# Kernel tuning notes

Hardware: AMD Instinct MI355X
Metric: run time of the kernel (lower is better)

Reference implementation:

```python
import jax, jax.numpy as jnp
import numpy as np

N_NODES = 50000
N_EDGES = 1_600_000
IN_DIM = 64
HID_DIM = 64
OUT_DIM = 64


def setup_inputs() -> dict:
    key = jax.random.key(0)
    k = jax.random.split(key, 7)
    feat = jax.random.normal(k[0], (N_NODES, IN_DIM), dtype=jnp.float32)
    src = jax.random.randint(k[1], (N_EDGES,), 0, N_NODES, dtype=jnp.int32)
    dst = jax.random.randint(k[2], (N_EDGES,), 0, N_NODES, dtype=jnp.int32)
    # nn.init.normal_(weight, std=0.1); bias default uniform ~ small, use 0.1*randn
    W1 = 0.1 * jax.random.normal(k[3], (HID_DIM, IN_DIM), dtype=jnp.float32)
    b1 = 0.1 * jax.random.normal(k[4], (HID_DIM,), dtype=jnp.float32)
    W2 = 0.1 * jax.random.normal(k[5], (OUT_DIM, HID_DIM), dtype=jnp.float32)
    b2 = 0.1 * jax.random.normal(k[6], (OUT_DIM,), dtype=jnp.float32)
    return {"feat": feat, "src": src, "dst": dst, "W1": W1, "b1": b1, "W2": W2, "b2": b2}


def _gnn_layer(h, src, dst, W, b):
    # copy_u + sum: gather source-node features along edges, scatter-sum to dst
    agg = jax.ops.segment_sum(h[src], dst, num_segments=N_NODES)  # [N, d_in]
    return agg @ W.T + b  # nn.Linear


def reference(feat, src, dst, W1, b1, W2, b2):
    h = _gnn_layer(feat, src, dst, W1, b1)
    h = jnp.tanh(h)
    h = _gnn_layer(h, src, dst, W2, b2)
    return h
```

## Files before the change

kernel.cpp:

```cpp
#include <hip/hip_runtime.h>

#define N_NODES 50000
#define N_EDGES 1600000
#define DIM 64
#define NBK 196
#define BIN_BLOCKS 391
#define CSR_CAP 12288
#define QCAP 3072

__device__ __forceinline__ unsigned short f2bf(float f) {
    union { float f; unsigned u; } v; v.f = f;
    unsigned r = v.u + 0x7FFF + ((v.u >> 16) & 1);
    return (unsigned short)(r >> 16);
}
__device__ __forceinline__ float bf2f(unsigned short h) {
    union { unsigned u; float f; } v; v.u = ((unsigned)h) << 16;
    return v.f;
}

__global__ __launch_bounds__(256) void init_bcur(int* __restrict__ bcur) {
    if (threadIdx.x < NBK) bcur[threadIdx.x * 16] = threadIdx.x * CSR_CAP;
}

__global__ __launch_bounds__(256) void bin_edges(const int* __restrict__ src,
                                                 const int* __restrict__ dst,
                                                 int* __restrict__ bcur,
                                                 int* __restrict__ binned) {
    __shared__ int cnt[NBK];
    __shared__ int lofs[NBK];
    __shared__ int shiftv[NBK];
    __shared__ int sb[256];
    __shared__ int stag[4096];
    __shared__ unsigned char stb[4096];
    int tid = threadIdx.x;
    if (tid < NBK) cnt[tid] = 0;
    __syncthreads();

    int base = blockIdx.x * 4096;
    int nedge = N_EDGES - base;
    if (nedge > 4096) nedge = 4096;

    int myb[16], myr[16], myp[16];
#pragma unroll
    for (int i = 0; i < 16; ++i) {
        int e = base + i * 256 + tid;
        myb[i] = -1;
        if (e < N_EDGES) {
            int s = src[e], d = dst[e];
            int b = d >> 8;
            myb[i] = b;
            myp[i] = ((d & 255) << 16) | s;
            myr[i] = atomicAdd(&cnt[b], 1);
        }
    }
    __syncthreads();

    int c = (tid < NBK) ? cnt[tid] : 0;
    sb[tid] = c;
    __syncthreads();
    for (int off = 1; off < 256; off <<= 1) {
        int u = (tid >= off) ? sb[tid - off] : 0;
        __syncthreads();
        sb[tid] += u;
        __syncthreads();
    }
    if (tid < NBK) {
        lofs[tid] = sb[tid] - c;
        if (c) shiftv[tid] = atomicAdd(&bcur[tid * 16], c) - lofs[tid];
    }
    __syncthreads();

#pragma unroll
    for (int i = 0; i < 16; ++i) {
        if (myb[i] >= 0) {
            int idx = lofs[myb[i]] + myr[i];
            stag[idx] = myp[i];
            stb[idx] = (unsigned char)myb[i];
        }
    }
    __syncthreads();

    for (int i = tid; i < nedge; i += 256)
        binned[i + shiftv[stb[i]]] = stag[i];
}

__global__ __launch_bounds__(256) void build_csr(const int* __restrict__ binned,
                                                 const int* __restrict__ bcur,
                                                 unsigned* __restrict__ nodeinfo,
                                                 unsigned short* __restrict__ csr16) {
    __shared__ int cnt[64], cnt2[64], ofs[64], pcs[64], sb[64];
    __shared__ int qtot;
    int tid = threadIdx.x;
    int b = blockIdx.x >> 2;
    int q = blockIdx.x & 3;
    int ibase = b * CSR_CAP;
    int qbase = (b * 4 + q) * QCAP;
    int m = bcur[b * 16] - ibase;
    if (m > CSR_CAP) m = CSR_CAP;
    if (tid < 64) { cnt[tid] = 0; cnt2[tid] = 0; }
    __syncthreads();

    for (int i = tid; i < m; i += 256) {
        int dl = (binned[ibase + i] >> 16) & 255;
        if ((dl >> 6) == q) atomicAdd(&cnt[dl & 63], 1);
    }
    __syncthreads();

    int v = 0;
    if (tid < 64) {
        v = (cnt[tid] + 7) & ~7;
        pcs[tid] = v;
        sb[tid] = v;
    }
    __syncthreads();
    for (int off = 1; off < 64; off <<= 1) {
        int u = (tid >= off && tid < 64) ? sb[tid - off] : 0;
        __syncthreads();
        if (tid < 64) sb[tid] += u;
        __syncthreads();
    }
    if (tid < 64) {
        ofs[tid] = sb[tid] - v;
        int node = (b << 8) + (q << 6) + tid;
        if (node < N_NODES)
            nodeinfo[node] = ((unsigned)v << 23) | (unsigned)(qbase + ofs[tid]);
    }
    if (tid == 63) qtot = sb[63];
    __syncthreads();

    int qt = qtot;
    for (int i = tid; i < qt; i += 256) csr16[qbase + i] = (unsigned short)N_NODES;
    __syncthreads();

    for (int i = tid; i < m; i += 256) {
        int p = binned[ibase + i];
        int dl = (p >> 16) & 255;
        if ((dl >> 6) == q) {
            int r = atomicAdd(&cnt2[dl & 63], 1);
            csr16[qbase + ofs[dl & 63] + r] = (unsigned short)(p & 0xFFFF);
        }
    }
}

__global__ __launch_bounds__(256) void gemm64_f32(const float* __restrict__ X,
                                                  const float* __restrict__ W,
                                                  unsigned short* __restrict__ T,
                                                  int n_rows) {
    __shared__ float Ws[64 * 64];
    int tid = threadIdx.x;
#pragma unroll
    for (int j = 0; j < 16; ++j) Ws[j * 256 + tid] = W[j * 256 + tid];
    __syncthreads();

    int n = blockIdx.x * 256 + tid;
    if (n >= n_rows) {
        if (n == n_rows) {
            ushort4 z = {0, 0, 0, 0};
            ushort4* tp = (ushort4*)(T + (size_t)n * 64);
#pragma unroll
            for (int k = 0; k < 16; ++k) tp[k] = z;
        }
        return;
    }

    float4 x[16];
    const float4* xp = (const float4*)(X + (size_t)n * 64);
#pragma unroll
    for (int k = 0; k < 16; ++k) x[k] = xp[k];

    ushort4* tp = (ushort4*)(T + (size_t)n * 64);
    for (int fg = 0; fg < 16; ++fg) {
        float r[4];
#pragma unroll
        for (int fi = 0; fi < 4; ++fi) {
            int f = fg * 4 + fi;
            float acc = 0.f;
#pragma unroll
            for (int k4 = 0; k4 < 16; ++k4) {
                float4 w = *(const float4*)&Ws[f * 64 + k4 * 4];
                float4 xv = x[k4];
                acc += xv.x * w.x + xv.y * w.y + xv.z * w.z + xv.w * w.w;
            }
            r[fi] = acc;
        }
        ushort4 o;
        o.x = f2bf(r[0]); o.y = f2bf(r[1]); o.z = f2bf(r[2]); o.w = f2bf(r[3]);
        tp[fg] = o;
    }
}

__global__ __launch_bounds__(256) void gemm64_bf16(const unsigned short* __restrict__ X,
                                                   const float* __restrict__ W,
                                                   unsigned short* __restrict__ T,
                                                   int n_rows) {
    __shared__ float Ws[64 * 64];
    int tid = threadIdx.x;
#pragma unroll
    for (int j = 0; j < 16; ++j) Ws[j * 256 + tid] = W[j * 256 + tid];
    __syncthreads();

    int n = blockIdx.x * 256 + tid;
    if (n >= n_rows) {
        if (n == n_rows) {
            ushort4 z = {0, 0, 0, 0};
            ushort4* tp = (ushort4*)(T + (size_t)n * 64);
#pragma unroll
            for (int k = 0; k < 16; ++k) tp[k] = z;
        }
        return;
    }

    uint4 xr[8];
    const uint4* xp = (const uint4*)(X + (size_t)n * 64);
#pragma unroll
    for (int k = 0; k < 8; ++k) xr[k] = xp[k];
    float x[64];
    const unsigned* xu = (const unsigned*)xr;
#pragma unroll
    for (int p = 0; p < 32; ++p) {
        unsigned u = xu[p];
        union { unsigned u; float f; } lo, hi;
        lo.u = u << 16;
        hi.u = u & 0xFFFF0000u;
        x[2 * p] = lo.f;
        x[2 * p + 1] = hi.f;
    }

    const float4* xv4 = (const float4*)x;
    ushort4* tp = (ushort4*)(T + (size_t)n * 64);
    for (int fg = 0; fg < 16; ++fg) {
        float r[4];
#pragma unroll
        for (int fi = 0; fi < 4; ++fi) {
            int f = fg * 4 + fi;
            float acc = 0.f;
#pragma unroll
            for (int k4 = 0; k4 < 16; ++k4) {
                float4 w = *(const float4*)&Ws[f * 64 + k4 * 4];
                float4 xv = xv4[k4];
                acc += xv.x * w.x + xv.y * w.y + xv.z * w.z + xv.w * w.w;
            }
            r[fi] = acc;
        }
        ushort4 o;
        o.x = f2bf(r[0]); o.y = f2bf(r[1]); o.z = f2bf(r[2]); o.w = f2bf(r[3]);
        tp[fg] = o;
    }
}

__global__ __launch_bounds__(256) void aggregate(const unsigned short* __restrict__ T,
                                                 const unsigned short* __restrict__ csr,
                                                 const unsigned* __restrict__ nodeinfo,
                                                 const float* __restrict__ bias,
                                                 void* __restrict__ outp,
                                                 int mode) {
    int node = blockIdx.x * 4 + (threadIdx.x >> 6);
    int lane = threadIdx.x & 63;
    if (node >= N_NODES) return;
    unsigned info = nodeinfo[node];
    int pos = (int)(info & 0x7FFFFFu);
    int pcnt = (int)(info >> 23);
    const uint4* ix = (const uint4*)(csr + pos);
    float acc = bias[lane];
    int groups = pcnt >> 3;
    if (groups) {
        uint4 iv = ix[0];
        for (int g = 0; g < groups; ++g) {
            uint4 ivn;
            if (g + 1 < groups) ivn = ix[g + 1];
            int s0 = iv.x & 0xFFFF, s1 = iv.x >> 16;
            int s2 = iv.y & 0xFFFF, s3 = iv.y >> 16;
            int s4 = iv.z & 0xFFFF, s5 = iv.z >> 16;
            int s6 = iv.w & 0xFFFF, s7 = iv.w >> 16;
            unsigned short v0 = T[(size_t)s0 * DIM + lane];
            unsigned short v1 = T[(size_t)s1 * DIM + lane];
            unsigned short v2 = T[(size_t)s2 * DIM + lane];
            unsigned short v3 = T[(size_t)s3 * DIM + lane];
            unsigned short v4 = T[(size_t)s4 * DIM + lane];
            unsigned short v5 = T[(size_t)s5 * DIM + lane];
            unsigned short v6 = T[(size_t)s6 * DIM + lane];
            unsigned short v7 = T[(size_t)s7 * DIM + lane];
            acc += (bf2f(v0) + bf2f(v1)) + (bf2f(v2) + bf2f(v3)) +
                   (bf2f(v4) + bf2f(v5)) + (bf2f(v6) + bf2f(v7));
            iv = ivn;
        }
    }
    if (mode) {
        float e = __expf(2.f * acc);
        acc = 1.f - 2.f / (e + 1.f);
        ((unsigned short*)outp)[(size_t)node * DIM + lane] = f2bf(acc);
    } else {
        ((float*)outp)[(size_t)node * DIM + lane] = acc;
    }
}

extern "C" void kernel_launch(void* const* d_in, const int* in_sizes, int n_in,
                              void* d_out, int out_size, void* d_ws, size_t ws_size,
                              hipStream_t stream) {
    const float* feat = (const float*)d_in[0];
    const int*   src  = (const int*)d_in[1];
    const int*   dst  = (const int*)d_in[2];
    const float* W1   = (const float*)d_in[3];
    const float* b1   = (const float*)d_in[4];
    const float* W2   = (const float*)d_in[5];
    const float* b2   = (const float*)d_in[6];

    int*            binned   = (int*)d_ws;
    unsigned short* csr16    = (unsigned short*)(binned + NBK * CSR_CAP);
    unsigned*       nodeinfo = (unsigned*)(csr16 + NBK * CSR_CAP);
    int*            bcur     = (int*)(nodeinfo + N_NODES);
    unsigned short* t        = (unsigned short*)(bcur + NBK * 16 + 8);

    unsigned short* h = (unsigned short*)d_out;
    float* out = (float*)d_out;

    const int NB = (N_NODES + 3) / 4;
    const int GB = (N_NODES + 256) / 256;

    init_bcur<<<1, 256, 0, stream>>>(bcur);
    bin_edges<<<BIN_BLOCKS, 256, 0, stream>>>(src, dst, bcur, binned);
    build_csr<<<NBK * 4, 256, 0, stream>>>(binned, bcur, nodeinfo, csr16);

    gemm64_f32<<<GB, 256, 0, stream>>>(feat, W1, t, N_NODES);
    aggregate<<<NB, 256, 0, stream>>>(t, csr16, nodeinfo, b1, h, 1);

    gemm64_bf16<<<GB, 256, 0, stream>>>(h, W2, t, N_NODES);
    aggregate<<<NB, 256, 0, stream>>>(t, csr16, nodeinfo, b2, out, 0);
}
```

Measured before the change: 252.6 us.

## Use 64-node CSR buckets and 16-byte vector gathers in aggregation

Edge binning now uses 782 buckets of 64 destination nodes instead of 196 buckets of 256, so build_csr runs one block per bucket and no longer scans each bucket four times with a quarter filter. The aggregate kernel now has each group of 8 lanes gather a full 16-byte slice of one source row, covering 8 edges at once, and then reduces across lanes with xor shuffles. This replaces eight 2-byte scalar loads per lane with one vector load, cutting memory transactions per edge at the cost of shuffle reductions. The workspace is reordered so the feature table comes first, which keeps its rows 16-byte aligned.

```diff
diff --git a/kernel.cpp b/kernel.cpp
--- a/kernel.cpp
+++ b/kernel.cpp
@@ -3,79 +3,99 @@
 #define N_NODES 50000
 #define N_EDGES 1600000
 #define DIM 64
-#define NBK 196
-#define BIN_BLOCKS 391
-#define CSR_CAP 12288
-#define QCAP 3072
+#define SBK 782
+#define SCAP 2560
+#define BIN_EPB 2048
+#define BIN_BLOCKS 782
 
 __device__ __forceinline__ unsigned short f2bf(float f) {
     union { float f; unsigned u; } v; v.f = f;
     unsigned r = v.u + 0x7FFF + ((v.u >> 16) & 1);
     return (unsigned short)(r >> 16);
 }
-__device__ __forceinline__ float bf2f(unsigned short h) {
-    union { unsigned u; float f; } v; v.u = ((unsigned)h) << 16;
-    return v.f;
+__device__ __forceinline__ float bf_lo(unsigned u) {
+    union { unsigned u; float f; } v; v.u = u << 16;  return v.f;
+}
+__device__ __forceinline__ float bf_hi(unsigned u) {
+    union { unsigned u; float f; } v; v.u = u & 0xFFFF0000u;  return v.f;
 }
 
 __global__ __launch_bounds__(256) void init_bcur(int* __restrict__ bcur) {
-    if (threadIdx.x < NBK) bcur[threadIdx.x * 16] = threadIdx.x * CSR_CAP;
+    for (int i = threadIdx.x; i < SBK; i += 256) bcur[i * 16] = i * SCAP;
 }
 
 __global__ __launch_bounds__(256) void bin_edges(const int* __restrict__ src,
                                                  const int* __restrict__ dst,
                                                  int* __restrict__ bcur,
                                                  int* __restrict__ binned) {
-    __shared__ int cnt[NBK];
-    __shared__ int lofs[NBK];
-    __shared__ int shiftv[NBK];
-    __shared__ int sb[256];
-    __shared__ int stag[4096];
-    __shared__ unsigned char stb[4096];
+    __shared__ int cnt[SBK];
+    __shared__ int lofs[SBK];
+    __shared__ int shiftv[SBK];
+    __shared__ int csum[256];
+    __shared__ int stag[BIN_EPB];
+    __shared__ unsigned short stb[BIN_EPB];
     int tid = threadIdx.x;
-    if (tid < NBK) cnt[tid] = 0;
-    __syncthreads();
-
-    int base = blockIdx.x * 4096;
+    for (int i = tid; i < SBK; i += 256) cnt[i] = 0;
+    __syncthreads();
+
+    int base = blockIdx.x * BIN_EPB;
     int nedge = N_EDGES - base;
-    if (nedge > 4096) nedge = 4096;
-
-    int myb[16], myr[16], myp[16];
-#pragma unroll
-    for (int i = 0; i < 16; ++i) {
+    if (nedge > BIN_EPB) nedge = BIN_EPB;
+
+    int myb[8], myr[8], myp[8];
+#pragma unroll
+    for (int i = 0; i < 8; ++i) {
         int e = base + i * 256 + tid;
         myb[i] = -1;
         if (e < N_EDGES) {
             int s = src[e], d = dst[e];
-            int b = d >> 8;
+            int b = d >> 6;
             myb[i] = b;
-            myp[i] = ((d & 255) << 16) | s;
+            myp[i] = ((d & 63) << 16) | s;
             myr[i] = atomicAdd(&cnt[b], 1);
         }
     }
     __syncthreads();
 
-    int c = (tid < NBK) ? cnt[tid] : 0;
-    sb[tid] = c;
+    int c4[4] = {0, 0, 0, 0};
+    int own = 0;
+    if (tid < 196) {
+#pragma unroll
+        for (int j = 0; j < 4; ++j) {
+            int idx = tid * 4 + j;
+            if (idx < SBK) { c4[j] = cnt[idx]; own += c4[j]; }
+        }
+    }
+    csum[tid] = own;
     __syncthreads();
     for (int off = 1; off < 256; off <<= 1) {
-        int u = (tid >= off) ? sb[tid - off] : 0;
+        int u = (tid >= off) ? csum[tid - off] : 0;
         __syncthreads();
-        sb[tid] += u;
+        csum[tid] += u;
         __syncthreads();
     }
-    if (tid < NBK) {
-        lofs[tid] = sb[tid] - c;
-        if (c) shiftv[tid] = atomicAdd(&bcur[tid * 16], c) - lofs[tid];
-    }
-    __syncthreads();
-
-#pragma unroll
-    for (int i = 0; i < 16; ++i) {
+    if (tid < 196) {
+        int run = csum[tid] - own;
+#pragma unroll
+        for (int j = 0; j < 4; ++j) {
+            int idx = tid * 4 + j;
+            if (idx < SBK) { lofs[idx] = run; run += c4[j]; }
+        }
+    }
+    __syncthreads();
+
+    for (int i = tid; i < SBK; i += 256) {
+        int c = cnt[i];
+        if (c) shiftv[i] = atomicAdd(&bcur[i * 16], c) - lofs[i];
+    }
+    __syncthreads();
+
+#pragma unroll
+    for (int i = 0; i < 8; ++i) {
         if (myb[i] >= 0) {
             int idx = lofs[myb[i]] + myr[i];
             stag[idx] = myp[i];
-            stb[idx] = (unsigned char)myb[i];
+            stb[idx] = (unsigned short)myb[i];
         }
     }
     __syncthreads();
@@ -88,30 +108,22 @@
                                                  const int* __restrict__ bcur,
                                                  unsigned* __restrict__ nodeinfo,
                                                  unsigned short* __restrict__ csr16) {
-    __shared__ int cnt[64], cnt2[64], ofs[64], pcs[64], sb[64];
+    __shared__ int cnt[64], cnt2[64], ofs[64], sb[64];
     __shared__ int qtot;
     int tid = threadIdx.x;
-    int b = blockIdx.x >> 2;
-    int q = blockIdx.x & 3;
-    int ibase = b * CSR_CAP;
-    int qbase = (b * 4 + q) * QCAP;
+    int b = blockIdx.x;
+    int ibase = b * SCAP;
     int m = bcur[b * 16] - ibase;
-    if (m > CSR_CAP) m = CSR_CAP;
+    if (m > SCAP) m = SCAP;
     if (tid < 64) { cnt[tid] = 0; cnt2[tid] = 0; }
     __syncthreads();
 
-    for (int i = tid; i < m; i += 256) {
-        int dl = (binned[ibase + i] >> 16) & 255;
-        if ((dl >> 6) == q) atomicAdd(&cnt[dl & 63], 1);
-    }
+    for (int i = tid; i < m; i += 256)
+        atomicAdd(&cnt[binned[ibase + i] >> 16], 1);
     __syncthreads();
 
     int v = 0;
-    if (tid < 64) {
-        v = (cnt[tid] + 7) & ~7;
-        pcs[tid] = v;
-        sb[tid] = v;
-    }
+    if (tid < 64) { v = (cnt[tid] + 7) & ~7; sb[tid] = v; }
     __syncthreads();
     for (int off = 1; off < 64; off <<= 1) {
         int u = (tid >= off && tid < 64) ? sb[tid - off] : 0;
@@ -121,24 +133,22 @@
     }
     if (tid < 64) {
         ofs[tid] = sb[tid] - v;
-        int node = (b << 8) + (q << 6) + tid;
+        int node = (b << 6) + tid;
         if (node < N_NODES)
-            nodeinfo[node] = ((unsigned)v << 23) | (unsigned)(qbase + ofs[tid]);
+            nodeinfo[node] = ((unsigned)v << 22) | (unsigned)(ibase + ofs[tid]);
     }
     if (tid == 63) qtot = sb[63];
     __syncthreads();
 
     int qt = qtot;
-    for (int i = tid; i < qt; i += 256) csr16[qbase + i] = (unsigned short)N_NODES;
+    for (int i = tid; i < qt; i += 256) csr16[ibase + i] = (unsigned short)N_NODES;
     __syncthreads();
 
     for (int i = tid; i < m; i += 256) {
         int p = binned[ibase + i];
-        int dl = (p >> 16) & 255;
-        if ((dl >> 6) == q) {
-            int r = atomicAdd(&cnt2[dl & 63], 1);
-            csr16[qbase + ofs[dl & 63] + r] = (unsigned short)(p & 0xFFFF);
-        }
+        int dl = p >> 16;
+        int r = atomicAdd(&cnt2[dl], 1);
+        csr16[ibase + ofs[dl] + r] = (unsigned short)(p & 0xFFFF);
     }
 }
 
@@ -219,11 +229,8 @@
 #pragma unroll
     for (int p = 0; p < 32; ++p) {
         unsigned u = xu[p];
-        union { unsigned u; float f; } lo, hi;
-        lo.u = u << 16;
-        hi.u = u & 0xFFFF0000u;
-        x[2 * p] = lo.f;
-        x[2 * p + 1] = hi.f;
+        x[2 * p] = bf_lo(u);
+        x[2 * p + 1] = bf_hi(u);
     }
 
     const float4* xv4 = (const float4*)x;
@@ -258,39 +265,52 @@
     int lane = threadIdx.x & 63;
     if (node >= N_NODES) return;
     unsigned info = nodeinfo[node];
-    int pos = (int)(info & 0x7FFFFFu);
-    int pcnt = (int)(info >> 23);
+    int pos = (int)(info & 0x3FFFFFu);
+    int groups = (int)(info >> 22) >> 3;
+    int q = lane >> 3;
+    int fl = lane & 7;
     const uint4* ix = (const uint4*)(csr + pos);
-    float acc = bias[lane];
-    int groups = pcnt >> 3;
+    const char* Tb = (const char*)T;
+    int fb = fl * 16;
+
+    float a0 = 0.f, a1 = 0.f, a2 = 0.f, a3 = 0.f,
+          a4 = 0.f, a5 = 0.f, a6 = 0.f, a7 = 0.f;
     if (groups) {
         uint4 iv = ix[0];
         for (int g = 0; g < groups; ++g) {
             uint4 ivn;
             if (g + 1 < groups) ivn = ix[g + 1];
-            int s0 = iv.x & 0xFFFF, s1 = iv.x >> 16;
-            int s2 = iv.y & 0xFFFF, s3 = iv.y >> 16;
-            int s4 = iv.z & 0xFFFF, s5 = iv.z >> 16;
-            int s6 = iv.w & 0xFFFF, s7 = iv.w >> 16;
-            unsigned short v0 = T[(size_t)s0 * DIM + lane];
-            unsigned short v1 = T[(size_t)s1 * DIM + lane];
-            unsigned short v2 = T[(size_t)s2 * DIM + lane];
-            unsigned short v3 = T[(size_t)s3 * DIM + lane];
-            unsigned short v4 = T[(size_t)s4 * DIM + lane];
-            unsigned short v5 = T[(size_t)s5 * DIM + lane];
-            unsigned short v6 = T[(size_t)s6 * DIM + lane];
-            unsigned short v7 = T[(size_t)s7 * DIM + lane];
-            acc += (bf2f(v0) + bf2f(v1)) + (bf2f(v2) + bf2f(v3)) +
-                   (bf2f(v4) + bf2f(v5)) + (bf2f(v6) + bf2f(v7));
+            unsigned w = (q & 2) ? ((q & 4) ? iv.w : iv.y)
+                                 : ((q & 4) ? iv.z : iv.x);
+            unsigned s = (q & 1) ? (w >> 16) : (w & 0xFFFFu);
+            uint4 r = *(const uint4*)(Tb + (size_t)s * 128 + fb);
+            a0 += bf_lo(r.x); a1 += bf_hi(r.x);
+            a2 += bf_lo(r.y); a3 += bf_hi(r.y);
+            a4 += bf_lo(r.z); a5 += bf_hi(r.z);
+            a6 += bf_lo(r.w); a7 += bf_hi(r.w);
             iv = ivn;
         }
     }
+#pragma unroll
+    for (int mask = 8; mask <= 32; mask <<= 1) {
+        a0 += __shfl_xor(a0, mask, 64);
+        a1 += __shfl_xor(a1, mask, 64);
+        a2 += __shfl_xor(a2, mask, 64);
+        a3 += __shfl_xor(a3, mask, 64);
+        a4 += __shfl_xor(a4, mask, 64);
+        a5 += __shfl_xor(a5, mask, 64);
+        a6 += __shfl_xor(a6, mask, 64);
+        a7 += __shfl_xor(a7, mask, 64);
+    }
+    int col = fl * 8 + q;
+    float av[8] = {a0, a1, a2, a3, a4, a5, a6, a7};
+    float a = av[q] + bias[col];
     if (mode) {
-        float e = __expf(2.f * acc);
-        acc = 1.f - 2.f / (e + 1.f);
-        ((unsigned short*)outp)[(size_t)node * DIM + lane] = f2bf(acc);
+        float e = __expf(2.f * a);
+        a = 1.f - 2.f / (e + 1.f);
+        ((unsigned short*)outp)[(size_t)node * DIM + col] = f2bf(a);
     } else {
-        ((float*)outp)[(size_t)node * DIM + lane] = acc;
+        ((float*)outp)[(size_t)node * DIM + col] = a;
     }
 }
 
@@ -305,11 +325,11 @@
     const float* W2   = (const float*)d_in[5];
     const float* b2   = (const float*)d_in[6];
 
-    int*            binned   = (int*)d_ws;
-    unsigned short* csr16    = (unsigned short*)(binned + NBK * CSR_CAP);
-    unsigned*       nodeinfo = (unsigned*)(csr16 + NBK * CSR_CAP);
+    unsigned short* t        = (unsigned short*)d_ws;
+    int*            binned   = (int*)(t + (size_t)(N_NODES + 1) * 64);
+    unsigned short* csr16    = (unsigned short*)(binned + SBK * SCAP);
+    unsigned*       nodeinfo = (unsigned*)(csr16 + SBK * SCAP);
     int*            bcur     = (int*)(nodeinfo + N_NODES);
-    unsigned short* t        = (unsigned short*)(bcur + NBK * 16 + 8);
 
     unsigned short* h = (unsigned short*)d_out;
     float* out = (float*)d_out;
@@ -319,7 +339,7 @@
 
     init_bcur<<<1, 256, 0, stream>>>(bcur);
     bin_edges<<<BIN_BLOCKS, 256, 0, stream>>>(src, dst, bcur, binned);
-    build_csr<<<NBK * 4, 256, 0, stream>>>(binned, bcur, nodeinfo, csr16);
+    build_csr<<<SBK, 256, 0, stream>>>(binned, bcur, nodeinfo, csr16);
 
     gemm64_f32<<<GB, 256, 0, stream>>>(feat, W1, t, N_NODES);
     aggregate<<<NB, 256, 0, stream>>>(t, csr16, nodeinfo, b1, h, 1);
```

Result: slower. 266.6 us (+5.5%).

## Gather 16-byte feature chunks per lane in aggregate and reduce via wave shuffles

Applied to the files above, without the earlier changes.

The aggregate kernel now assigns each lane one of the 8 edges in a group and one 16-byte slice of the source row, so each lane does a single uint4 load instead of eight scalar 2-byte loads. Partial sums for the 8 features in that slice are combined across edge lanes with xor shuffles, and then each lane picks one output column. The aim is to cut the number of memory instructions and make gather loads wider, at the cost of shuffle reductions and a strided output column mapping. The workspace offset for nodeinfo is also corrected to match the csr16 size, and an unused shared array is removed.

```diff
diff --git a/kernel.cpp b/kernel.cpp
--- a/kernel.cpp
+++ b/kernel.cpp
@@ -13,9 +13,11 @@
     unsigned r = v.u + 0x7FFF + ((v.u >> 16) & 1);
     return (unsigned short)(r >> 16);
 }
-__device__ __forceinline__ float bf2f(unsigned short h) {
-    union { unsigned u; float f; } v; v.u = ((unsigned)h) << 16;
-    return v.f;
+__device__ __forceinline__ float bf_lo(unsigned u) {
+    union { unsigned u; float f; } v; v.u = u << 16;  return v.f;
+}
+__device__ __forceinline__ float bf_hi(unsigned u) {
+    union { unsigned u; float f; } v; v.u = u & 0xFFFF0000u;  return v.f;
 }
 
 __global__ __launch_bounds__(256) void init_bcur(int* __restrict__ bcur) {
@@ -88,7 +90,7 @@
                                                  const int* __restrict__ bcur,
                                                  unsigned* __restrict__ nodeinfo,
                                                  unsigned short* __restrict__ csr16) {
-    __shared__ int cnt[64], cnt2[64], ofs[64], pcs[64], sb[64];
+    __shared__ int cnt[64], cnt2[64], ofs[64], sb[64];
     __shared__ int qtot;
     int tid = threadIdx.x;
     int b = blockIdx.x >> 2;
@@ -107,11 +109,7 @@
     __syncthreads();
 
     int v = 0;
-    if (tid < 64) {
-        v = (cnt[tid] + 7) & ~7;
-        pcs[tid] = v;
-        sb[tid] = v;
-    }
+    if (tid < 64) { v = (cnt[tid] + 7) & ~7; sb[tid] = v; }
     __syncthreads();
     for (int off = 1; off < 64; off <<= 1) {
         int u = (tid >= off && tid < 64) ? sb[tid - off] : 0;
@@ -219,11 +217,8 @@
 #pragma unroll
     for (int p = 0; p < 32; ++p) {
         unsigned u = xu[p];
-        union { unsigned u; float f; } lo, hi;
-        lo.u = u << 16;
-        hi.u = u & 0xFFFF0000u;
-        x[2 * p] = lo.f;
-        x[2 * p + 1] = hi.f;
+        x[2 * p] = bf_lo(u);
+        x[2 * p + 1] = bf_hi(u);
     }
 
     const float4* xv4 = (const float4*)x;
@@ -259,38 +254,52 @@
     if (node >= N_NODES) return;
     unsigned info = nodeinfo[node];
     int pos = (int)(info & 0x7FFFFFu);
-    int pcnt = (int)(info >> 23);
+    int groups = (int)(info >> 23) >> 3;
+    int q = lane >> 3;
+    int fl = lane & 7;
     const uint4* ix = (const uint4*)(csr + pos);
-    float acc = bias[lane];
-    int groups = pcnt >> 3;
+    const char* Tb = (const char*)T;
+    int fb = fl * 16;
+
+    float a0 = 0.f, a1 = 0.f, a2 = 0.f, a3 = 0.f,
+          a4 = 0.f, a5 = 0.f, a6 = 0.f, a7 = 0.f;
     if (groups) {
         uint4 iv = ix[0];
         for (int g = 0; g < groups; ++g) {
             uint4 ivn;
             if (g + 1 < groups) ivn = ix[g + 1];
-            int s0 = iv.x & 0xFFFF, s1 = iv.x >> 16;
-            int s2 = iv.y & 0xFFFF, s3 = iv.y >> 16;
-            int s4 = iv.z & 0xFFFF, s5 = iv.z >> 16;
-            int s6 = iv.w & 0xFFFF, s7 = iv.w >> 16;
-            unsigned short v0 = T[(size_t)s0 * DIM + lane];
-            unsigned short v1 = T[(size_t)s1 * DIM + lane];
-            unsigned short v2 = T[(size_t)s2 * DIM + lane];
-            unsigned short v3 = T[(size_t)s3 * DIM + lane];
-            unsigned short v4 = T[(size_t)s4 * DIM + lane];
-            unsigned short v5 = T[(size_t)s5 * DIM + lane];
-            unsigned short v6 = T[(size_t)s6 * DIM + lane];
-            unsigned short v7 = T[(size_t)s7 * DIM + lane];
-            acc += (bf2f(v0) + bf2f(v1)) + (bf2f(v2) + bf2f(v3)) +
-                   (bf2f(v4) + bf2f(v5)) + (bf2f(v6) + bf2f(v7));
+            unsigned w = (q & 2) ? ((q & 4) ? iv.w : iv.y)
+                                 : ((q & 4) ? iv.z : iv.x);
+            unsigned s = (q & 1) ? (w >> 16) : (w & 0xFFFFu);
+            uint4 r = *(const uint4*)(Tb + (size_t)s * 128 + fb);
+            a0 += bf_lo(r.x); a1 += bf_hi(r.x);
+            a2 += bf_lo(r.y); a3 += bf_hi(r.y);
+            a4 += bf_lo(r.z); a5 += bf_hi(r.z);
+            a6 += bf_lo(r.w); a7 += bf_hi(r.w);
             iv = ivn;
         }
     }
+#pragma unroll
+    for (int mask = 8; mask <= 32; mask <<= 1) {
+        a0 += __shfl_xor(a0, mask, 64);
+        a1 += __shfl_xor(a1, mask, 64);
+        a2 += __shfl_xor(a2, mask, 64);
+        a3 += __shfl_xor(a3, mask, 64);
+        a4 += __shfl_xor(a4, mask, 64);
+        a5 += __shfl_xor(a5, mask, 64);
+        a6 += __shfl_xor(a6, mask, 64);
+        a7 += __shfl_xor(a7, mask, 64);
+    }
+    float a = (q < 4) ? ((q < 2) ? (q == 0 ? a0 : a1) : (q == 2 ? a2 : a3))
+                      : ((q < 6) ? (q == 4 ? a4 : a5) : (q == 6 ? a6 : a7));
+    int col = fl * 8 + q;
+    a += bias[col];
     if (mode) {
-        float e = __expf(2.f * acc);
-        acc = 1.f - 2.f / (e + 1.f);
-        ((unsigned short*)outp)[(size_t)node * DIM + lane] = f2bf(acc);
+        float e = __expf(2.f * a);
+        a = 1.f - 2.f / (e + 1.f);
+        ((unsigned short*)outp)[(size_t)node * DIM + col] = f2bf(a);
     } else {
-        ((float*)outp)[(size_t)node * DIM + lane] = acc;
+        ((float*)outp)[(size_t)node * DIM + col] = a;
     }
 }
 
@@ -307,7 +316,7 @@
 
     int*            binned   = (int*)d_ws;
     unsigned short* csr16    = (unsigned short*)(binned + NBK * CSR_CAP);
-    unsigned*       nodeinfo = (unsigned*)(csr16 + NBK * CSR_CAP);
+    unsigned*       nodeinfo = (unsigned*)(csr16 + NBK * 4 * QCAP);
     int*            bcur     = (int*)(nodeinfo + N_NODES);
     unsigned short* t        = (unsigned short*)(bcur + NBK * 16 + 8);
 
```

Measured after the change: 259.9 us. +2.9%, slower.

## Fuse edge binning with first GEMM and unroll aggregation by sixteen edges

Applied to the files above, without the earlier changes.

Merges the edge-binning kernel and the first feature GEMM into one launch, with extra blocks taking the GEMM role, so the two independent stages run concurrently. The bcur init kernel becomes a memset, with the bin base offset added inside the kernel. Node edge lists are padded to multiples of 16 so the aggregation loop can issue 16 gathers per iteration into two accumulators, raising memory-level parallelism. The fused kernel's shared memory grows by the 16KB weight tile for all blocks, which may lower occupancy of the binning blocks, and padding adds more dummy gathers.

```diff
diff --git a/kernel.cpp b/kernel.cpp
--- a/kernel.cpp
+++ b/kernel.cpp
@@ -7,32 +7,80 @@
 #define BIN_BLOCKS 391
 #define CSR_CAP 12288
 #define QCAP 3072
+#define GEMM_BLOCKS 197
 
 __device__ __forceinline__ unsigned short f2bf(float f) {
     union { float f; unsigned u; } v; v.f = f;
     unsigned r = v.u + 0x7FFF + ((v.u >> 16) & 1);
     return (unsigned short)(r >> 16);
 }
+__device__ __forceinline__ float bf_lo(unsigned u) {
+    union { unsigned u; float f; } v; v.u = u << 16;  return v.f;
+}
+__device__ __forceinline__ float bf_hi(unsigned u) {
+    union { unsigned u; float f; } v; v.u = u & 0xFFFF0000u;  return v.f;
+}
 __device__ __forceinline__ float bf2f(unsigned short h) {
-    union { unsigned u; float f; } v; v.u = ((unsigned)h) << 16;
-    return v.f;
-}
-
-__global__ __launch_bounds__(256) void init_bcur(int* __restrict__ bcur) {
-    if (threadIdx.x < NBK) bcur[threadIdx.x * 16] = threadIdx.x * CSR_CAP;
-}
-
-__global__ __launch_bounds__(256) void bin_edges(const int* __restrict__ src,
-                                                 const int* __restrict__ dst,
-                                                 int* __restrict__ bcur,
-                                                 int* __restrict__ binned) {
+    union { unsigned u; float f; } v; v.u = ((unsigned)h) << 16;  return v.f;
+}
+
+__global__ __launch_bounds__(256) void bin_and_gemm1(const int* __restrict__ src,
+                                                     const int* __restrict__ dst,
+                                                     int* __restrict__ bcur,
+                                                     int* __restrict__ binned,
+                                                     const float* __restrict__ X,
+                                                     const float* __restrict__ W,
+                                                     unsigned short* __restrict__ T) {
     __shared__ int cnt[NBK];
     __shared__ int lofs[NBK];
     __shared__ int shiftv[NBK];
     __shared__ int sb[256];
     __shared__ int stag[4096];
     __shared__ unsigned char stb[4096];
+    __shared__ float Ws[64 * 64];
     int tid = threadIdx.x;
+
+    if (blockIdx.x >= BIN_BLOCKS) {
+#pragma unroll
+        for (int j = 0; j < 16; ++j) Ws[j * 256 + tid] = W[j * 256 + tid];
+        __syncthreads();
+
+        int n = (blockIdx.x - BIN_BLOCKS) * 256 + tid;
+        if (n > N_NODES) return;
+        ushort4* tp = (ushort4*)(T + (size_t)n * 64);
+        if (n == N_NODES) {
+            ushort4 z = {0, 0, 0, 0};
+#pragma unroll
+            for (int k = 0; k < 16; ++k) tp[k] = z;
+            return;
+        }
+
+        float4 x[16];
+        const float4* xp = (const float4*)(X + (size_t)n * 64);
+#pragma unroll
+        for (int k = 0; k < 16; ++k) x[k] = xp[k];
+
+        for (int fg = 0; fg < 16; ++fg) {
+            float r[4];
+#pragma unroll
+            for (int fi = 0; fi < 4; ++fi) {
+                int f = fg * 4 + fi;
+                float acc = 0.f;
+#pragma unroll
+                for (int k4 = 0; k4 < 16; ++k4) {
+                    float4 w = *(const float4*)&Ws[f * 64 + k4 * 4];
+                    float4 xv = x[k4];
+                    acc += xv.x * w.x + xv.y * w.y + xv.z * w.z + xv.w * w.w;
+                }
+                r[fi] = acc;
+            }
+            ushort4 o;
+            o.x = f2bf(r[0]); o.y = f2bf(r[1]); o.z = f2bf(r[2]); o.w = f2bf(r[3]);
+            tp[fg] = o;
+        }
+        return;
+    }
+
     if (tid < NBK) cnt[tid] = 0;
     __syncthreads();
 
@@ -66,7 +114,7 @@
     }
     if (tid < NBK) {
         lofs[tid] = sb[tid] - c;
-        if (c) shiftv[tid] = atomicAdd(&bcur[tid * 16], c) - lofs[tid];
+        if (c) shiftv[tid] = tid * CSR_CAP + atomicAdd(&bcur[tid * 16], c) - lofs[tid];
     }
     __syncthreads();
 
@@ -88,14 +136,14 @@
                                                  const int* __restrict__ bcur,
                                                  unsigned* __restrict__ nodeinfo,
                                                  unsigned short* __restrict__ csr16) {
-    __shared__ int cnt[64], cnt2[64], ofs[64], pcs[64], sb[64];
+    __shared__ int cnt[64], cnt2[64], ofs[64], sb[64];
     __shared__ int qtot;
     int tid = threadIdx.x;
     int b = blockIdx.x >> 2;
     int q = blockIdx.x & 3;
     int ibase = b * CSR_CAP;
     int qbase = (b * 4 + q) * QCAP;
-    int m = bcur[b * 16] - ibase;
+    int m = bcur[b * 16];
     if (m > CSR_CAP) m = CSR_CAP;
     if (tid < 64) { cnt[tid] = 0; cnt2[tid] = 0; }
     __syncthreads();
@@ -107,11 +155,7 @@
     __syncthreads();
 
     int v = 0;
-    if (tid < 64) {
-        v = (cnt[tid] + 7) & ~7;
-        pcs[tid] = v;
-        sb[tid] = v;
-    }
+    if (tid < 64) { v = (cnt[tid] + 15) & ~15; sb[tid] = v; }
     __syncthreads();
     for (int off = 1; off < 64; off <<= 1) {
         int u = (tid >= off && tid < 64) ? sb[tid - off] : 0;
@@ -142,53 +186,6 @@
     }
 }
 
-__global__ __launch_bounds__(256) void gemm64_f32(const float* __restrict__ X,
-                                                  const float* __restrict__ W,
-                                                  unsigned short* __restrict__ T,
-                                                  int n_rows) {
-    __shared__ float Ws[64 * 64];
-    int tid = threadIdx.x;
-#pragma unroll
-    for (int j = 0; j < 16; ++j) Ws[j * 256 + tid] = W[j * 256 + tid];
-    __syncthreads();
-
-    int n = blockIdx.x * 256 + tid;
-    if (n >= n_rows) {
-        if (n == n_rows) {
-            ushort4 z = {0, 0, 0, 0};
-            ushort4* tp = (ushort4*)(T + (size_t)n * 64);
-#pragma unroll
-            for (int k = 0; k < 16; ++k) tp[k] = z;
-        }
-        return;
-    }
-
-    float4 x[16];
-    const float4* xp = (const float4*)(X + (size_t)n * 64);
-#pragma unroll
-    for (int k = 0; k < 16; ++k) x[k] = xp[k];
-
-    ushort4* tp = (ushort4*)(T + (size_t)n * 64);
-    for (int fg = 0; fg < 16; ++fg) {
-        float r[4];
-#pragma unroll
-        for (int fi = 0; fi < 4; ++fi) {
-            int f = fg * 4 + fi;
-            float acc = 0.f;
-#pragma unroll
-            for (int k4 = 0; k4 < 16; ++k4) {
-                float4 w = *(const float4*)&Ws[f * 64 + k4 * 4];
-                float4 xv = x[k4];
-                acc += xv.x * w.x + xv.y * w.y + xv.z * w.z + xv.w * w.w;
-            }
-            r[fi] = acc;
-        }
-        ushort4 o;
-        o.x = f2bf(r[0]); o.y = f2bf(r[1]); o.z = f2bf(r[2]); o.w = f2bf(r[3]);
-        tp[fg] = o;
-    }
-}
-
 __global__ __launch_bounds__(256) void gemm64_bf16(const unsigned short* __restrict__ X,
                                                    const float* __restrict__ W,
                                                    unsigned short* __restrict__ T,
@@ -219,11 +216,8 @@
 #pragma unroll
     for (int p = 0; p < 32; ++p) {
         unsigned u = xu[p];
-        union { unsigned u; float f; } lo, hi;
-        lo.u = u << 16;
-        hi.u = u & 0xFFFF0000u;
-        x[2 * p] = lo.f;
-        x[2 * p + 1] = hi.f;
+        x[2 * p] = bf_lo(u);
+        x[2 * p + 1] = bf_hi(u);
     }
 
     const float4* xv4 = (const float4*)x;
@@ -259,32 +253,43 @@
     if (node >= N_NODES) return;
     unsigned info = nodeinfo[node];
     int pos = (int)(info & 0x7FFFFFu);
-    int pcnt = (int)(info >> 23);
+    int groups = (int)(info >> 23) >> 3;
     const uint4* ix = (const uint4*)(csr + pos);
     float acc = bias[lane];
-    int groups = pcnt >> 3;
-    if (groups) {
-        uint4 iv = ix[0];
-        for (int g = 0; g < groups; ++g) {
-            uint4 ivn;
-            if (g + 1 < groups) ivn = ix[g + 1];
-            int s0 = iv.x & 0xFFFF, s1 = iv.x >> 16;
-            int s2 = iv.y & 0xFFFF, s3 = iv.y >> 16;
-            int s4 = iv.z & 0xFFFF, s5 = iv.z >> 16;
-            int s6 = iv.w & 0xFFFF, s7 = iv.w >> 16;
-            unsigned short v0 = T[(size_t)s0 * DIM + lane];
-            unsigned short v1 = T[(size_t)s1 * DIM + lane];
-            unsigned short v2 = T[(size_t)s2 * DIM + lane];
-            unsigned short v3 = T[(size_t)s3 * DIM + lane];
-            unsigned short v4 = T[(size_t)s4 * DIM + lane];
-            unsigned short v5 = T[(size_t)s5 * DIM + lane];
-            unsigned short v6 = T[(size_t)s6 * DIM + lane];
-            unsigned short v7 = T[(size_t)s7 * DIM + lane];
-            acc += (bf2f(v0) + bf2f(v1)) + (bf2f(v2) + bf2f(v3)) +
-                   (bf2f(v4) + bf2f(v5)) + (bf2f(v6) + bf2f(v7));
-            iv = ivn;
-        }
-    }
+    float acc2 = 0.f;
+    for (int g = 0; g < groups; g += 2) {
+        uint4 ia = ix[g];
+        uint4 ib = ix[g + 1];
+        int s0 = ia.x & 0xFFFF, s1 = ia.x >> 16;
+        int s2 = ia.y & 0xFFFF, s3 = ia.y >> 16;
+        int s4 = ia.z & 0xFFFF, s5 = ia.z >> 16;
+        int s6 = ia.w & 0xFFFF, s7 = ia.w >> 16;
+        int u0 = ib.x & 0xFFFF, u1 = ib.x >> 16;
+        int u2 = ib.y & 0xFFFF, u3 = ib.y >> 16;
+        int u4 = ib.z & 0xFFFF, u5 = ib.z >> 16;
+        int u6 = ib.w & 0xFFFF, u7 = ib.w >> 16;
+        unsigned short v0 = T[(size_t)s0 * DIM + lane];
+        unsigned short v1 = T[(size_t)s1 * DIM + lane];
+        unsigned short v2 = T[(size_t)s2 * DIM + lane];
+        unsigned short v3 = T[(size_t)s3 * DIM + lane];
+        unsigned short v4 = T[(size_t)s4 * DIM + lane];
+        unsigned short v5 = T[(size_t)s5 * DIM + lane];
+        unsigned short v6 = T[(size_t)s6 * DIM + lane];
+        unsigned short v7 = T[(size_t)s7 * DIM + lane];
+        unsigned short w0 = T[(size_t)u0 * DIM + lane];
+        unsigned short w1 = T[(size_t)u1 * DIM + lane];
+        unsigned short w2 = T[(size_t)u2 * DIM + lane];
+        unsigned short w3 = T[(size_t)u3 * DIM + lane];
+        unsigned short w4 = T[(size_t)u4 * DIM + lane];
+        unsigned short w5 = T[(size_t)u5 * DIM + lane];
+        unsigned short w6 = T[(size_t)u6 * DIM + lane];
+        unsigned short w7 = T[(size_t)u7 * DIM + lane];
+        acc  += (bf2f(v0) + bf2f(v1)) + (bf2f(v2) + bf2f(v3)) +
+                (bf2f(v4) + bf2f(v5)) + (bf2f(v6) + bf2f(v7));
+        acc2 += (bf2f(w0) + bf2f(w1)) + (bf2f(w2) + bf2f(w3)) +
+                (bf2f(w4) + bf2f(w5)) + (bf2f(w6) + bf2f(w7));
+    }
+    acc += acc2;
     if (mode) {
         float e = __expf(2.f * acc);
         acc = 1.f - 2.f / (e + 1.f);
@@ -307,7 +312,7 @@
 
     int*            binned   = (int*)d_ws;
     unsigned short* csr16    = (unsigned short*)(binned + NBK * CSR_CAP);
-    unsigned*       nodeinfo = (unsigned*)(csr16 + NBK * CSR_CAP);
+    unsigned*       nodeinfo = (unsigned*)(csr16 + NBK * 4 * QCAP);
     int*            bcur     = (int*)(nodeinfo + N_NODES);
     unsigned short* t        = (unsigned short*)(bcur + NBK * 16 + 8);
 
@@ -315,15 +320,14 @@
     float* out = (float*)d_out;
 
     const int NB = (N_NODES + 3) / 4;
-    const int GB = (N_NODES + 256) / 256;
-
-    init_bcur<<<1, 256, 0, stream>>>(bcur);
-    bin_edges<<<BIN_BLOCKS, 256, 0, stream>>>(src, dst, bcur, binned);
+
+    hipMemsetAsync(bcur, 0, NBK * 16 * sizeof(int), stream);
+    bin_and_gemm1<<<BIN_BLOCKS + GEMM_BLOCKS, 256, 0, stream>>>(
+        src, dst, bcur, binned, feat, W1, t);
     build_csr<<<NBK * 4, 256, 0, stream>>>(binned, bcur, nodeinfo, csr16);
 
-    gemm64_f32<<<GB, 256, 0, stream>>>(feat, W1, t, N_NODES);
     aggregate<<<NB, 256, 0, stream>>>(t, csr16, nodeinfo, b1, h, 1);
 
-    gemm64_bf16<<<GB, 256, 0, stream>>>(h, W2, t, N_NODES);
+    gemm64_bf16<<<GEMM_BLOCKS, 256, 0, stream>>>(h, W2, t, N_NODES);
     aggregate<<<NB, 256, 0, stream>>>(t, csr16, nodeinfo, b2, out, 0);
 }
```

Result: faster. 243.9 us (-3.5%).
